# Kernel optimization log

Measured on AMD Instinct MI355X. Metric: run time of the kernel, lower is better.

Reference implementation:

```python
import jax, jax.numpy as jnp
import numpy as np

K = 20
EPS = 1e-5  # BatchNorm eps; eval mode with running_mean=0, running_var=1


def _lrelu(x):
    return jnp.where(x >= 0, x, 0.2 * x)


def _bn(x, g, b):
    # eval-mode BN (fresh running stats: mean=0, var=1); channel axis = 1
    shape = (1, -1) + (1,) * (x.ndim - 2)
    return x * (g / jnp.sqrt(1.0 + EPS)).reshape(shape) + b.reshape(shape)


def _knn_idx(x, k):
    # x: (B, C, N). Negative squared euclidean distance, top-k = nearest.
    xx = jnp.sum(x * x, axis=1)                      # (B, N)
    inner = jnp.einsum('bcn,bcm->bnm', x, x)         # (B, N, N)
    neg_d = 2.0 * inner - xx[:, :, None] - xx[:, None, :]
    return jax.lax.top_k(neg_d, k)[1]                # (B, N, K)


def _gather(x, idx):
    # x: (B, C, N), idx: (B, N, K) -> (B, C, N, K)
    return jax.vmap(lambda xb, ib: xb[:, ib])(x, idx)


def setup_inputs() -> dict:
    key = jax.random.key(0)
    ks = jax.random.split(key, 32)
    B, N = 8, 2048
    d = {}
    d['x'] = jax.random.normal(ks[0], (B, 3, N), jnp.float32)

    def w(k_, o, i):
        return jax.random.normal(k_, (o, i), jnp.float32) * (1.0 / np.sqrt(i))

    d['W1'] = w(ks[1], 64, 3)
    d['W2'] = w(ks[2], 64, 64)
    d['W3'] = w(ks[3], 128, 64)
    d['W4'] = w(ks[4], 256, 128)
    d['W5'] = w(ks[5], 1024, 512)
    bn_dims = [64, 64, 128, 256, 1024, 512, 256]
    for i, c in enumerate(bn_dims):
        d[f'g{i+1}'] = 1.0 + 0.1 * jax.random.normal(ks[6 + 2 * i], (c,), jnp.float32)
        d[f'b{i+1}'] = 0.1 * jax.random.normal(ks[7 + 2 * i], (c,), jnp.float32)
    d['L1W'] = w(ks[20], 512, 2048)
    d['L2W'] = w(ks[21], 256, 512)
    d['L2b'] = 0.1 * jax.random.normal(ks[22], (256,), jnp.float32)
    d['L3W'] = w(ks[23], 40, 256)
    d['L3b'] = 0.1 * jax.random.normal(ks[24], (40,), jnp.float32)
    return d


def reference(x, W1, W2, W3, W4, W5,
              g1, b1, g2, b2, g3, b3, g4, b4, g5, b5, g6, b6, g7, b7,
              L1W, L2W, L2b, L3W, L3b):
    idx = _knn_idx(x, K)  # shared neighbor indices for all EdgeConv blocks

    h = _lrelu(_bn(jnp.einsum('oc,bcnk->bonk', W1, _gather(x, idx)), g1, b1))
    x1 = h.max(axis=-1)                               # (B, 64, N)
    h = _lrelu(_bn(jnp.einsum('oc,bcnk->bonk', W2, _gather(x1, idx)), g2, b2))
    x2 = h.max(axis=-1)                               # (B, 64, N)
    h = _lrelu(_bn(jnp.einsum('oc,bcnk->bonk', W3, _gather(x2, idx)), g3, b3))
    x3 = h.max(axis=-1)                               # (B, 128, N)
    h = _lrelu(_bn(jnp.einsum('oc,bcnk->bonk', W4, _gather(x3, idx)), g4, b4))
    x4 = h.max(axis=-1)                               # (B, 256, N)

    cat = jnp.concatenate([x1, x2, x3, x4], axis=1)   # (B, 512, N)
    h = _lrelu(_bn(jnp.einsum('oc,bcn->bon', W5, cat), g5, b5))  # (B, 1024, N)

    f = jnp.concatenate([h.max(axis=-1), h.mean(axis=-1)], axis=1)  # (B, 2048)
    f = _lrelu(_bn(f @ L1W.T, g6, b6))
    f = _lrelu(_bn(f @ L2W.T + L2b, g7, b7))          # dropout is identity in eval
    return f @ L3W.T + L3b                            # (B, 40)
```

## Files before the change

kernel.cpp:

```cpp
#include <hip/hip_runtime.h>
#include <math.h>


#define WS_IDX      0
#define WS_Y16      1310720
#define WS_XCAT16   9699328
#define WS_W16      26476544
#define WS_FMAX     27615232
#define WS_FSUM     27648000
#define WS_A1       27680768
#define WS_A2       27697152

typedef _Float16 f16x8 __attribute__((ext_vector_type(8)));
typedef float f32x4 __attribute__((ext_vector_type(4)));

struct F3 { float x, y, z; };

__device__ __forceinline__ float lrelu(float v) { return (v >= 0.f) ? v : 0.2f * v; }
__device__ __forceinline__ unsigned sortable_f32(float f) {
  unsigned b = __float_as_uint(f);
  return b ^ (((unsigned)((int)b >> 31)) | 0x80000000u);
}
__device__ __forceinline__ float desort_f32(unsigned u) {
  unsigned b = (u & 0x80000000u) ? (u ^ 0x80000000u) : ~u;
  return __uint_as_float(b);
}

__global__ __launch_bounds__(256) void knn_prep_kernel(
    const float* __restrict__ x, const float* __restrict__ W1,
    const float* __restrict__ g1, const float* __restrict__ b1,
    const float* __restrict__ W2, const float* __restrict__ W3,
    const float* __restrict__ W4, const float* __restrict__ W5,
    _Float16* __restrict__ w16, unsigned* __restrict__ fzero,
    int* __restrict__ idxo, _Float16* __restrict__ xcat) {
  __shared__ F3 pts_s[2048];
  __shared__ unsigned long long cand_s[8][60];
  __shared__ unsigned cnt_s[8];
  __shared__ int sel_s[8][20];
  int tid = threadIdx.x;

  if (blockIdx.x >= 2048) {
    int bid = blockIdx.x - 2048;
#pragma unroll
    for (int t = 0; t < 8; ++t) {
      int i = bid * 2048 + t * 256 + tid;
      if (i < 4096) w16[i] = (_Float16)W2[i];
      else if (i < 12288) w16[i] = (_Float16)W3[i - 4096];
      else if (i < 45056) w16[i] = (_Float16)W4[i - 12288];
      else if (i < 569344) w16[i] = (_Float16)W5[i - 45056];
      else fzero[i - 569344] = 0u;
    }
    return;
  }

  int lwave = tid >> 6, lane = tid & 63;
  int qbase = blockIdx.x * 8;
  int b = qbase >> 11;
  int nbase = qbase & 2047;
  const float* xb = x + b * 6144;
#pragma unroll
  for (int i = 0; i < 8; ++i) {
    int m = tid + i * 256;
    F3 p; p.x = xb[m]; p.y = xb[2048 + m]; p.z = xb[4096 + m];
    pts_s[m] = p;
  }
  if (lane == 0) cnt_s[lwave * 2] = 0, cnt_s[lwave * 2 + 1] = 0;
  __syncthreads();

  F3 q[2];
  float qw[2];
  unsigned keys[2][32];
  unsigned lmax[2] = {0u, 0u};
#pragma unroll
  for (int qi = 0; qi < 2; ++qi) {
    q[qi] = pts_s[nbase + lwave * 2 + qi];
    qw[qi] = q[qi].x * q[qi].x + q[qi].y * q[qi].y + q[qi].z * q[qi].z;
  }
#pragma unroll
  for (int j = 0; j < 32; ++j) {
    F3 p = pts_s[j * 64 + lane];
    float pw = p.x * p.x + p.y * p.y + p.z * p.z;
#pragma unroll
    for (int qi = 0; qi < 2; ++qi) {
      float nd = 2.0f * (q[qi].x * p.x + q[qi].y * p.y + q[qi].z * p.z) -
                 qw[qi] - pw;
      unsigned key = sortable_f32(nd);
      keys[qi][j] = key;
      lmax[qi] = (key > lmax[qi]) ? key : lmax[qi];
    }
  }
  unsigned lo[2] = {0u, 0u}, hi[2] = {0x8001u, 0x8001u};
  for (int it = 0; it < 16; ++it) {
#pragma unroll
    for (int qi = 0; qi < 2; ++qi) {
      unsigned mid = (lo[qi] + hi[qi] + 1) >> 1;
      int cnt = __popcll(__ballot(lmax[qi] >= (mid << 16)));
      if (cnt >= 20) lo[qi] = mid; else hi[qi] = mid;
    }
  }
  unsigned T[2] = {lo[0] << 16, lo[1] << 16};
#pragma unroll
  for (int j = 0; j < 32; ++j) {
    int m = j * 64 + lane;
#pragma unroll
    for (int qi = 0; qi < 2; ++qi) {
      unsigned key = keys[qi][j];
      if (key >= T[qi]) {
        unsigned pos = atomicAdd(&cnt_s[lwave * 2 + qi], 1u);
        if (pos < 60)
          cand_s[lwave * 2 + qi][pos] =
              (((unsigned long long)key) << 32) | (unsigned)(2047 - m);
      }
    }
  }
#pragma unroll
  for (int qi = 0; qi < 2; ++qi) {
    int qq = lwave * 2 + qi;
    int row = qbase + qq;
    int outb = row * 20;
    unsigned C = cnt_s[qq];
    if (C <= 60) {
      unsigned long long v = (lane < (int)C) ? ~cand_s[qq][lane] : ~0ull;
#pragma unroll
      for (int k = 2; k <= 64; k <<= 1) {
#pragma unroll
        for (int jj = k >> 1; jj > 0; jj >>= 1) {
          unsigned long long o = __shfl_xor(v, jj, 64);
          bool lower = (lane & jj) == 0;
          bool up = (lane & k) == 0;
          bool takeMin = (lower == up);
          bool sw = takeMin ? (o < v) : (o > v);
          v = sw ? o : v;
        }
      }
      if (lane < 20) {
        unsigned long long pack = ~v;
        int m = 2047 - (int)(pack & 0xFFFFFFFFu);
        idxo[outb + lane] = m;
        sel_s[qq][lane] = m;
      }
    } else {
      unsigned long long prev = ~0ull;
      for (int r = 0; r < 20; ++r) {
        unsigned long long best = 0ull;
#pragma unroll
        for (int j = 0; j < 32; ++j) {
          int m = j * 64 + lane;
          unsigned long long pk =
              (((unsigned long long)keys[qi][j]) << 32) |
              (unsigned)(2047 - m);
          bool ok = (pk < prev) & (pk > best);
          best = ok ? pk : best;
        }
#pragma unroll
        for (int off = 1; off < 64; off <<= 1) {
          unsigned long long o = __shfl_xor(best, off, 64);
          best = (o > best) ? o : best;
        }
        int m = 2047 - (int)(best & 0xFFFFFFFFu);
        if (lane == 0) { idxo[outb + r] = m; sel_s[qq][r] = m; }
        prev = best;
      }
    }
  }
  float w0 = W1[lane * 3 + 0], w1 = W1[lane * 3 + 1], w2 = W1[lane * 3 + 2];
  float inv = 1.0f / sqrtf(1.0f + 1e-5f);
  float sc = g1[lane] * inv, bi = b1[lane];
#pragma unroll
  for (int qi = 0; qi < 2; ++qi) {
    int qq = lwave * 2 + qi;
    int row = qbase + qq;
    float mx = -3.4e38f, mn = 3.4e38f;
#pragma unroll
    for (int k = 0; k < 20; ++k) {
      F3 p = pts_s[sel_s[qq][k]];
      float v = w0 * p.x + w1 * p.y + w2 * p.z;
      mx = fmaxf(mx, v);
      mn = fminf(mn, v);
    }
    float v = (sc >= 0.0f) ? mx : mn;
    xcat[row * 512 + lane] = (_Float16)lrelu(sc * v + bi);
  }
}

template <int C, int COFF>
__global__ __launch_bounds__(256) void gmax_kernel(const _Float16* __restrict__ y,
                                                   const int* __restrict__ idx,
                                                   const float* __restrict__ g,
                                                   const float* __restrict__ bb,
                                                   _Float16* __restrict__ xcat) {
  constexpr int TP = C / 8;
  int e = blockIdx.x * 256 + threadIdx.x;
  int c8 = e & (TP - 1);
  int pg = e / TP;
  int b = pg >> 11;
  const int* ix = idx + pg * 20;
  int mm[20];
#pragma unroll
  for (int k = 0; k < 20; ++k) mm[k] = ix[k];
  int base = b * 2048 * C + c8 * 8;
  float mx[8], mn[8];
#pragma unroll
  for (int i = 0; i < 8; ++i) { mx[i] = -3.4e38f; mn[i] = 3.4e38f; }
#pragma unroll
  for (int k = 0; k < 20; ++k) {
    f16x8 v = *(const f16x8*)&y[base + mm[k] * C];
#pragma unroll
    for (int i = 0; i < 8; ++i) {
      float f = (float)v[i];
      mx[i] = fmaxf(mx[i], f);
      mn[i] = fminf(mn[i], f);
    }
  }
  float inv = 1.0f / sqrtf(1.0f + 1e-5f);
  f16x8 outv;
#pragma unroll
  for (int i = 0; i < 8; ++i) {
    float s = g[c8 * 8 + i] * inv;
    float v = (s >= 0.0f) ? mx[i] : mn[i];
    outv[i] = (_Float16)lrelu(s * v + bb[c8 * 8 + i]);
  }
  *(f16x8*)&xcat[pg * 512 + COFF + c8 * 8] = outv;
}

template <int CIN, int COUT, int XOFF>
__global__ __launch_bounds__(256) void gemm_mfma(const _Float16* __restrict__ Wh,
                                                 const _Float16* __restrict__ Xc,
                                                 _Float16* __restrict__ Y) {
  constexpr int BN = (COUT < 128) ? COUT : 128;
  constexpr int MT = (BN == 128) ? 4 : 2;
  __shared__ _Float16 Xs[128 * 40];
  __shared__ _Float16 Ws[BN * 40];
  int tid = threadIdx.x;
  int lane = tid & 63, w = tid >> 6;
  int wm = (BN == 128) ? (w & 1) : w;
  int wn = (BN == 128) ? (w >> 1) : 0;
  int col = lane & 15, quad = lane >> 4;
  int pg0 = blockIdx.x * 128;
  int o0 = blockIdx.y * BN;
  int r0 = tid >> 2;
  int c8 = (tid & 3) * 8;
  f32x4 acc[MT][4] = {};
  for (int k0 = 0; k0 < CIN; k0 += 32) {
    f16x8 xa = *(const f16x8*)&Xc[(pg0 + r0) * 512 + XOFF + k0 + c8];
    f16x8 xb2 = *(const f16x8*)&Xc[(pg0 + r0 + 64) * 512 + XOFF + k0 + c8];
    f16x8 wa = *(const f16x8*)&Wh[(o0 + r0) * CIN + k0 + c8];
    f16x8 wb;
    if (BN == 128) wb = *(const f16x8*)&Wh[(o0 + r0 + 64) * CIN + k0 + c8];
    __syncthreads();
    *(f16x8*)&Xs[r0 * 40 + c8] = xa;
    *(f16x8*)&Xs[(r0 + 64) * 40 + c8] = xb2;
    *(f16x8*)&Ws[r0 * 40 + c8] = wa;
    if (BN == 128) *(f16x8*)&Ws[(r0 + 64) * 40 + c8] = wb;
    __syncthreads();
    f16x8 af[MT], bf[4];
#pragma unroll
    for (int t = 0; t < MT; ++t)
      af[t] = *(const f16x8*)&Xs[(wm * (MT * 16) + t * 16 + col) * 40 + quad * 8];
#pragma unroll
    for (int t = 0; t < 4; ++t)
      bf[t] = *(const f16x8*)&Ws[(wn * 64 + t * 16 + col) * 40 + quad * 8];
#pragma unroll
    for (int mt = 0; mt < MT; ++mt)
#pragma unroll
      for (int nt = 0; nt < 4; ++nt)
        acc[mt][nt] = __builtin_amdgcn_mfma_f32_16x16x32_f16(af[mt], bf[nt],
                                                             acc[mt][nt], 0, 0, 0);
  }
#pragma unroll
  for (int mt = 0; mt < MT; ++mt)
#pragma unroll
    for (int nt = 0; nt < 4; ++nt)
#pragma unroll
      for (int r = 0; r < 4; ++r) {
        int p = pg0 + wm * (MT * 16) + mt * 16 + quad * 4 + r;
        int ch = o0 + wn * 64 + nt * 16 + col;
        Y[p * COUT + ch] = (_Float16)acc[mt][nt][r];
      }
}

typedef const __attribute__((address_space(1))) void* gas1_t;
typedef __attribute__((address_space(3))) void* las3_t;

__device__ __forceinline__ void stage16(const _Float16* g, char* l) {
  __builtin_amdgcn_global_load_lds((gas1_t)g, (las3_t)l, 16, 0, 0);
}

__global__ __launch_bounds__(512, 2) void gemm5_kernel(
    const _Float16* __restrict__ Wh, const _Float16* __restrict__ Xc,
    const float* __restrict__ g5, const float* __restrict__ b5,
    unsigned* __restrict__ fmax, float* __restrict__ fsum) {
  __shared__ __attribute__((aligned(16))) char lds[131072];
  char* ldsc = (char*)lds;
  const int tid = threadIdx.x;
  const int lane = tid & 63, w = tid >> 6;
  const int wm = w & 1, wn = w >> 1;
  const int col = lane & 15, quad = lane >> 4;
  const int pg0 = blockIdx.x * 256;
  const int o0 = blockIdx.y * 256;

  const int so = tid << 4;
  const int sl = so ^ (((so >> 9) & 3) << 5);
  const int srow0 = sl >> 7;
  const int skc0 = (sl & 127) >> 1;

#define STG(srcp, baserow, ktile, regoff, i)                                  \
  stage16((srcp) + ((baserow) + (i) * 64 + srow0) * 512 + (ktile) * 64 + skc0,\
          ldsc + (regoff) + (i) * 8192 + (w << 10))

  const int swc = ((col >> 2) & 3) << 5;
  const int labA = (col * 128 + quad * 16) ^ swc;
  const int labB = ((wn & 1) * 8192 + col * 128 + quad * 16) ^ swc;

#define RDA(m, kk) (*(const f16x8*)(rA + ((labA ^ ((kk) << 6)) + (m) * 2048)))
#define RDB(n, kk) (*(const f16x8*)(rB + ((labB ^ ((kk) << 6)) + (n) * 2048)))

  f32x4 acc[8][4] = {};

  STG(Wh, o0, 0, 32768, 0);       STG(Wh, o0, 0, 32768, 1);
  STG(Wh, o0 + 128, 0, 49152, 0); STG(Wh, o0 + 128, 0, 49152, 1);
  STG(Xc, pg0, 0, 0, 0);          STG(Xc, pg0 + 128, 0, 16384, 0);
  STG(Xc, pg0, 0, 0, 1);          STG(Xc, pg0 + 128, 0, 16384, 1);
  asm volatile("s_waitcnt vmcnt(0)" ::: "memory");
  __builtin_amdgcn_s_barrier();

  for (int t = 0; t < 8; ++t) {
    const int nt = t + 1;
    const char* rA = ldsc + (t & 1) * 65536 + wm * 16384;
    const char* rB = ldsc + (t & 1) * 65536 + 32768 + (wn >> 1) * 16384;
    const int nreg = (nt & 1) * 65536;
    f16x8 bf[4][2];
#pragma unroll
    for (int p = 0; p < 4; ++p) {
      f16x8 a[2][2];
#pragma unroll
      for (int mm = 0; mm < 2; ++mm)
#pragma unroll
        for (int kk = 0; kk < 2; ++kk)
          a[mm][kk] = RDA(2 * p + mm, kk);
      if (p == 0) {
#pragma unroll
        for (int n = 0; n < 4; ++n)
#pragma unroll
          for (int kk = 0; kk < 2; ++kk)
            bf[n][kk] = RDB(n, kk);
      }
      if (t < 7) {
        if (p == 0) { STG(Wh, o0, nt, nreg + 32768, 0);
                      STG(Wh, o0, nt, nreg + 32768, 1); }
        if (p == 1) { STG(Wh, o0 + 128, nt, nreg + 49152, 0);
                      STG(Wh, o0 + 128, nt, nreg + 49152, 1); }
        if (p == 2) { STG(Xc, pg0, nt, nreg + 0, 0);
                      STG(Xc, pg0 + 128, nt, nreg + 16384, 0); }
        if (p == 3) { STG(Xc, pg0, nt, nreg + 0, 1);
                      STG(Xc, pg0 + 128, nt, nreg + 16384, 1); }
      }
      if (p == 1) {
        if (t < 7) { asm volatile("s_waitcnt vmcnt(4)" ::: "memory"); }
        else       { asm volatile("s_waitcnt vmcnt(0)" ::: "memory"); }
      }
      if (p == 3 && t < 7) {
        asm volatile("s_waitcnt vmcnt(2)" ::: "memory");
      }
      __builtin_amdgcn_s_barrier();
      asm volatile("s_waitcnt lgkmcnt(0)" ::: "memory");
      __builtin_amdgcn_sched_barrier(0);
      __builtin_amdgcn_s_setprio(1);
#pragma unroll
      for (int mm = 0; mm < 2; ++mm)
#pragma unroll
        for (int n = 0; n < 4; ++n)
#pragma unroll
          for (int kk = 0; kk < 2; ++kk)
            acc[2 * p + mm][n] = __builtin_amdgcn_mfma_f32_16x16x32_f16(
                a[mm][kk], bf[n][kk], acc[2 * p + mm][n], 0, 0, 0);
      __builtin_amdgcn_s_setprio(0);
      __builtin_amdgcn_s_barrier();
    }
  }
#undef STG
#undef RDA
#undef RDB

  const float inv = 1.0f / sqrtf(1.0f + 1e-5f);
  const int b = pg0 >> 11;
#pragma unroll
  for (int n = 0; n < 4; ++n) {
    int ch = o0 + wn * 64 + n * 16 + col;
    float sc = g5[ch] * inv, bi = b5[ch];
    float mx = -3.4e38f, sm = 0.f;
#pragma unroll
    for (int m = 0; m < 8; ++m)
#pragma unroll
      for (int r = 0; r < 4; ++r) {
        float v = lrelu(acc[m][n][r] * sc + bi);
        mx = fmaxf(mx, v);
        sm += v;
      }
    mx = fmaxf(mx, __shfl_xor(mx, 16, 64));
    sm += __shfl_xor(sm, 16, 64);
    mx = fmaxf(mx, __shfl_xor(mx, 32, 64));
    sm += __shfl_xor(sm, 32, 64);
    if (quad == 0) {
      atomicMax(&fmax[b * 1024 + ch], sortable_f32(mx));
      atomicAdd(&fsum[b * 1024 + ch], sm);
    }
  }
}

__global__ __launch_bounds__(256) void l1_kernel(const unsigned* __restrict__ fmax,
                                                 const float* __restrict__ fsum,
                                                 const float* __restrict__ L1W,
                                                 const float* __restrict__ g6,
                                                 const float* __restrict__ b6,
                                                 float* __restrict__ a1) {
  int gw = (blockIdx.x * 256 + threadIdx.x) >> 6;
  int lane = threadIdx.x & 63;
  int b = gw >> 9, o = gw & 511;
  float s = 0.f;
#pragma unroll
  for (int i = 0; i < 32; ++i) {
    int j = lane + i * 64;
    float fj = (j < 1024) ? desort_f32(fmax[b * 1024 + j])
                          : fsum[b * 1024 + j - 1024] * (1.0f / 2048.0f);
    s += fj * L1W[o * 2048 + j];
  }
#pragma unroll
  for (int off = 1; off < 64; off <<= 1) s += __shfl_xor(s, off, 64);
  if (lane == 0) {
    float scv = g6[o] / sqrtf(1.0f + 1e-5f);
    a1[b * 512 + o] = lrelu(s * scv + b6[o]);
  }
}

__global__ __launch_bounds__(256) void l2_kernel(const float* __restrict__ a1,
                                                 const float* __restrict__ L2W,
                                                 const float* __restrict__ L2b,
                                                 const float* __restrict__ g7,
                                                 const float* __restrict__ b7,
                                                 float* __restrict__ a2) {
  int gw = (blockIdx.x * 256 + threadIdx.x) >> 6;
  int lane = threadIdx.x & 63;
  int b = gw >> 8, o = gw & 255;
  float s = 0.f;
#pragma unroll
  for (int i = 0; i < 8; ++i) {
    int j = lane + i * 64;
    s += a1[b * 512 + j] * L2W[o * 512 + j];
  }
#pragma unroll
  for (int off = 1; off < 64; off <<= 1) s += __shfl_xor(s, off, 64);
  if (lane == 0) {
    float v = s + L2b[o];
    float scv = g7[o] / sqrtf(1.0f + 1e-5f);
    a2[b * 256 + o] = lrelu(v * scv + b7[o]);
  }
}

__global__ __launch_bounds__(256) void l3_kernel(const float* __restrict__ a2,
                                                 const float* __restrict__ L3W,
                                                 const float* __restrict__ L3b,
                                                 float* __restrict__ out) {
  int gw = (blockIdx.x * 256 + threadIdx.x) >> 6;
  int lane = threadIdx.x & 63;
  int b = gw / 40, o = gw % 40;
  float s = 0.f;
#pragma unroll
  for (int i = 0; i < 4; ++i) {
    int j = lane + i * 64;
    s += a2[b * 256 + j] * L3W[o * 256 + j];
  }
#pragma unroll
  for (int off = 1; off < 64; off <<= 1) s += __shfl_xor(s, off, 64);
  if (lane == 0) out[b * 40 + o] = s + L3b[o];
}

extern "C" void kernel_launch(void* const* d_in, const int* in_sizes, int n_in,
                              void* d_out, int out_size, void* d_ws, size_t ws_size,
                              hipStream_t stream) {
  const float* x = (const float*)d_in[0];
  const float* W1 = (const float*)d_in[1];
  const float* W2 = (const float*)d_in[2];
  const float* W3 = (const float*)d_in[3];
  const float* W4 = (const float*)d_in[4];
  const float* W5 = (const float*)d_in[5];
  const float* g1 = (const float*)d_in[6];  const float* b1 = (const float*)d_in[7];
  const float* g2 = (const float*)d_in[8];  const float* b2 = (const float*)d_in[9];
  const float* g3 = (const float*)d_in[10]; const float* b3 = (const float*)d_in[11];
  const float* g4 = (const float*)d_in[12]; const float* b4 = (const float*)d_in[13];
  const float* g5 = (const float*)d_in[14]; const float* b5 = (const float*)d_in[15];
  const float* g6 = (const float*)d_in[16]; const float* b6 = (const float*)d_in[17];
  const float* g7 = (const float*)d_in[18]; const float* b7 = (const float*)d_in[19];
  const float* L1W = (const float*)d_in[20];
  const float* L2W = (const float*)d_in[21];
  const float* L2b = (const float*)d_in[22];
  const float* L3W = (const float*)d_in[23];
  const float* L3b = (const float*)d_in[24];

  char* w = (char*)d_ws;
  int* idxb = (int*)(w + WS_IDX);
  _Float16* y16 = (_Float16*)(w + WS_Y16);
  _Float16* xcat16 = (_Float16*)(w + WS_XCAT16);
  _Float16* w16 = (_Float16*)(w + WS_W16);
  unsigned* fmax = (unsigned*)(w + WS_FMAX);
  float* fsum = (float*)(w + WS_FSUM);
  float* a1 = (float*)(w + WS_A1);
  float* a2 = (float*)(w + WS_A2);

  knn_prep_kernel<<<2334, 256, 0, stream>>>(x, W1, g1, b1, W2, W3, W4, W5,
                                            w16, fmax, idxb, xcat16);
  gemm_mfma<64, 64, 0><<<dim3(128, 1), 256, 0, stream>>>(w16, xcat16, y16);
  gmax_kernel<64, 64><<<512, 256, 0, stream>>>(y16, idxb, g2, b2, xcat16);
  gemm_mfma<64, 128, 64><<<dim3(128, 1), 256, 0, stream>>>(w16 + 4096, xcat16, y16);
  gmax_kernel<128, 128><<<1024, 256, 0, stream>>>(y16, idxb, g3, b3, xcat16);
  gemm_mfma<128, 256, 128><<<dim3(128, 2), 256, 0, stream>>>(w16 + 12288, xcat16, y16);
  gmax_kernel<256, 256><<<2048, 256, 0, stream>>>(y16, idxb, g4, b4, xcat16);
  gemm5_kernel<<<dim3(64, 4), 512, 0, stream>>>(w16 + 45056, xcat16, g5, b5, fmax, fsum);
  l1_kernel<<<1024, 256, 0, stream>>>(fmax, fsum, L1W, g6, b6, a1);
  l2_kernel<<<512, 256, 0, stream>>>(a1, L2W, L2b, g7, b7, a2);
  l3_kernel<<<80, 256, 0, stream>>>(a2, L3W, L3b, (float*)d_out);
}
```

Before: 225.2 us.

## Fuse neighbor gather-max with following EdgeConv GEMM for layers 2 and 3

Adds a gemm_gather kernel that performs the k-NN gather, max/min selection, BN and leaky ReLU for a 128-point tile straight into LDS, then runs the next layer's MFMA GEMM on that tile. This replaces two gmax kernels and two separate GEMM launches, so the activations no longer take a round trip through global memory between those stages. A second Y buffer is added so the two fused kernels do not overwrite each other's input. For layer 3 the gather is done twice, once in each of the two y-blocks, which adds redundant gather work, and the weight staging has no double buffering.

```diff
diff --git a/kernel.cpp b/kernel.cpp
--- a/kernel.cpp
+++ b/kernel.cpp
@@ -10,6 +10,7 @@
 #define WS_FSUM     27648000
 #define WS_A1       27680768
 #define WS_A2       27697152
+#define WS_Y16B     27705344
 
 typedef _Float16 f16x8 __attribute__((ext_vector_type(8)));
 typedef float f32x4 __attribute__((ext_vector_type(4)));
@@ -279,6 +280,99 @@
       }
 }
 
+template <int CIN, int COUT, int XOFF>
+__global__ __launch_bounds__(256) void gemm_gather(
+    const _Float16* __restrict__ y, const int* __restrict__ idx,
+    const float* __restrict__ g, const float* __restrict__ bb,
+    const _Float16* __restrict__ Wh, _Float16* __restrict__ xcat,
+    _Float16* __restrict__ Yout) {
+  constexpr int BN = 128;
+  constexpr int MT = 4;
+  constexpr int CP = CIN + 8;
+  __shared__ _Float16 As[128 * CP];
+  __shared__ _Float16 Ws[BN * 40];
+  int tid = threadIdx.x;
+  int lane = tid & 63, w = tid >> 6;
+  int wm = w & 1, wn = w >> 1;
+  int col = lane & 15, quad = lane >> 4;
+  int pg0 = blockIdx.x * 128;
+  int o0 = blockIdx.y * BN;
+  const float inv = 1.0f / sqrtf(1.0f + 1e-5f);
+
+  constexpr int TPR = CIN / 8;
+#pragma unroll
+  for (int t = 0; t < (128 * TPR) / 256; ++t) {
+    int task = t * 256 + tid;
+    int r = task / TPR;
+    int c8 = task % TPR;
+    int pg = pg0 + r;
+    int b = pg >> 11;
+    const int* ix = idx + pg * 20;
+    int mm[20];
+#pragma unroll
+    for (int k = 0; k < 20; ++k) mm[k] = ix[k];
+    int base = b * 2048 * CIN + c8 * 8;
+    float mx[8], mn[8];
+#pragma unroll
+    for (int i = 0; i < 8; ++i) { mx[i] = -3.4e38f; mn[i] = 3.4e38f; }
+#pragma unroll
+    for (int k = 0; k < 20; ++k) {
+      f16x8 v = *(const f16x8*)&y[base + mm[k] * CIN];
+#pragma unroll
+      for (int i = 0; i < 8; ++i) {
+        float f = (float)v[i];
+        mx[i] = fmaxf(mx[i], f);
+        mn[i] = fminf(mn[i], f);
+      }
+    }
+    f16x8 outv;
+#pragma unroll
+    for (int i = 0; i < 8; ++i) {
+      float s = g[c8 * 8 + i] * inv;
+      float vv = (s >= 0.0f) ? mx[i] : mn[i];
+      outv[i] = (_Float16)lrelu(s * vv + bb[c8 * 8 + i]);
+    }
+    *(f16x8*)&As[r * CP + c8 * 8] = outv;
+    if (blockIdx.y == 0) *(f16x8*)&xcat[pg * 512 + XOFF + c8 * 8] = outv;
+  }
+  __syncthreads();
+
+  int r0 = tid >> 2;
+  int c8b = (tid & 3) * 8;
+  f32x4 acc[MT][4] = {};
+  for (int k0 = 0; k0 < CIN; k0 += 32) {
+    f16x8 wa = *(const f16x8*)&Wh[(o0 + r0) * CIN + k0 + c8b];
+    f16x8 wb = *(const f16x8*)&Wh[(o0 + r0 + 64) * CIN + k0 + c8b];
+    __syncthreads();
+    *(f16x8*)&Ws[r0 * 40 + c8b] = wa;
+    *(f16x8*)&Ws[(r0 + 64) * 40 + c8b] = wb;
+    __syncthreads();
+    f16x8 af[MT], bf[4];
+#pragma unroll
+    for (int t = 0; t < MT; ++t)
+      af[t] = *(const f16x8*)&As[(wm * 64 + t * 16 + col) * CP + k0 + quad * 8];
+#pragma unroll
+    for (int t = 0; t < 4; ++t)
+      bf[t] = *(const f16x8*)&Ws[(wn * 64 + t * 16 + col) * 40 + quad * 8];
+#pragma unroll
+    for (int mt = 0; mt < MT; ++mt)
+#pragma unroll
+      for (int nt = 0; nt < 4; ++nt)
+        acc[mt][nt] = __builtin_amdgcn_mfma_f32_16x16x32_f16(af[mt], bf[nt],
+                                                             acc[mt][nt], 0, 0, 0);
+  }
+#pragma unroll
+  for (int mt = 0; mt < MT; ++mt)
+#pragma unroll
+    for (int nt = 0; nt < 4; ++nt)
+#pragma unroll
+      for (int r = 0; r < 4; ++r) {
+        int p = pg0 + wm * 64 + mt * 16 + quad * 4 + r;
+        int ch = o0 + wn * 64 + nt * 16 + col;
+        Yout[p * COUT + ch] = (_Float16)acc[mt][nt][r];
+      }
+}
+
 typedef const __attribute__((address_space(1))) void* gas1_t;
 typedef __attribute__((address_space(3))) void* las3_t;
 
@@ -500,6 +594,7 @@
   char* w = (char*)d_ws;
   int* idxb = (int*)(w + WS_IDX);
   _Float16* y16 = (_Float16*)(w + WS_Y16);
+  _Float16* y16b = (_Float16*)(w + WS_Y16B);
   _Float16* xcat16 = (_Float16*)(w + WS_XCAT16);
   _Float16* w16 = (_Float16*)(w + WS_W16);
   unsigned* fmax = (unsigned*)(w + WS_FMAX);
@@ -510,10 +605,10 @@
   knn_prep_kernel<<<2334, 256, 0, stream>>>(x, W1, g1, b1, W2, W3, W4, W5,
                                             w16, fmax, idxb, xcat16);
   gemm_mfma<64, 64, 0><<<dim3(128, 1), 256, 0, stream>>>(w16, xcat16, y16);
-  gmax_kernel<64, 64><<<512, 256, 0, stream>>>(y16, idxb, g2, b2, xcat16);
-  gemm_mfma<64, 128, 64><<<dim3(128, 1), 256, 0, stream>>>(w16 + 4096, xcat16, y16);
-  gmax_kernel<128, 128><<<1024, 256, 0, stream>>>(y16, idxb, g3, b3, xcat16);
-  gemm_mfma<128, 256, 128><<<dim3(128, 2), 256, 0, stream>>>(w16 + 12288, xcat16, y16);
+  gemm_gather<64, 128, 64><<<dim3(128, 1), 256, 0, stream>>>(
+      y16, idxb, g2, b2, w16 + 4096, xcat16, y16b);
+  gemm_gather<128, 256, 128><<<dim3(128, 2), 256, 0, stream>>>(
+      y16b, idxb, g3, b3, w16 + 12288, xcat16, y16);
   gmax_kernel<256, 256><<<2048, 256, 0, stream>>>(y16, idxb, g4, b4, xcat16);
   gemm5_kernel<<<dim3(64, 4), 512, 0, stream>>>(w16 + 45056, xcat16, g5, b5, fmax, fsum);
   l1_kernel<<<1024, 256, 0, stream>>>(fmax, fsum, L1W, g6, b6, a1);
```

Result: no change. 225.5 us (+0.2%).
